# Performance work log

Measured on AMD Instinct MI355X. Metric: run time of the kernel, lower is better.

The kernel has to match this reference:

```python
import math
import jax, jax.numpy as jnp
import numpy as np

T_LEN, BATCH = 215, 256
D_INP = 36; D_MODEL = 36          # d_model must be 36 for internal dims to be consistent
D_T = D_MODEL + 36                # 72: transformer encoder width
N_HEAD = 4; D_HEAD = D_T // N_HEAD
D_FF = 128; N_LAYERS = 2; D_STATIC = 9; N_CLASSES = 2
N_NODES = 36

def _layer_norm(x, g, b, eps=1e-5):
    mu = jnp.mean(x, -1, keepdims=True)
    var = jnp.mean((x - mu) ** 2, -1, keepdims=True)
    return (x - mu) / jnp.sqrt(var + eps) * g + b

def _forward(src, static, times, lengths, W_enc, b_enc, W_emb, b_emb, Wq, bq, Wk, bk, Wv, bv, Wskip, bskip, enc_in_w, enc_in_b, enc_out_w, enc_out_b, enc_ff1_w, enc_ff1_b, enc_ff2_w, enc_ff2_b, enc_ln1_g, enc_ln1_b, enc_ln2_g, enc_ln2_b, mlp_w1, mlp_b1, mlp_w2, mlp_b2):
    T, B = src.shape[0], src.shape[1]
    x = (src[:, :, :D_INP] @ W_enc.T + b_enc) * math.sqrt(D_MODEL)          # [T,B,36]
    # positional encoding: 18 timescales = max_len ** linspace(0,1,18)
    timescales = jnp.asarray(215.0 ** np.linspace(0.0, 1.0, D_MODEL // 2), jnp.float32)
    scaled = times[:, :, None] / timescales                                  # [T,B,18]
    pe = jnp.concatenate([jnp.sin(scaled), jnp.cos(scaled)], -1)             # [T,B,36]
    emb = static @ W_emb.T + b_emb                                           # [B,36]
    mask = jnp.arange(T)[None, :] >= lengths[:, None]                        # [B,T] True = pad
    # --- batched TransformerConv over fully-connected 36-node graph (replaces per-sample loop) ---
    q = x @ Wq.T + bq; k = x @ Wk.T + bk; v = x @ Wv.T + bv
    skip = x @ Wskip.T + bskip
    scores = jnp.einsum('ibe,jbe->bij', q[:N_NODES], k[:N_NODES]) / math.sqrt(36.0)  # i=tgt, j=src
    A = jax.nn.softmax(scores, -1)                      # per-target softmax over incoming edges
    msg = jnp.einsum('bij,jbe->ibe', A, v[:N_NODES])    # edge_weights are all ones
    gout = skip.at[:N_NODES].add(msg)                   # [T,B,36]; rows >= 36 have no in-edges
    # per-edge alpha flattened in nonzero(adj) order: e = src*36 + tgt
    alpha_all = A.transpose(0, 2, 1).reshape(B, N_NODES * N_NODES).T         # [1296,B]
    sq = jnp.sum(alpha_all ** 2, 0)
    d2 = jnp.maximum(sq[:, None] + sq[None, :] - 2.0 * (alpha_all.T @ alpha_all), 0.0)
    distance = jnp.mean(jnp.sqrt(jnp.where(d2 > 0, d2, 1.0)) * (d2 > 0))     # mean pairwise L2
    # --- 2-layer post-norm transformer encoder, width 72, key padding mask ---
    h = jnp.concatenate([gout, pe], -1)                                      # [T,B,72]
    neg = jnp.where(mask[:, None, None, :], -1e9, 0.0)                       # [B,1,1,T]
    for l in range(N_LAYERS):
        qkv = h @ enc_in_w[l].T + enc_in_b[l]
        qh, kh, vh = [t.reshape(T, B, N_HEAD, D_HEAD) for t in jnp.split(qkv, 3, -1)]
        s = jnp.einsum('tbhd,sbhd->bhts', qh, kh) / math.sqrt(D_HEAD) + neg
        ctx = jnp.einsum('bhts,sbhd->tbhd', jax.nn.softmax(s, -1), vh).reshape(T, B, D_T)
        h = _layer_norm(h + ctx @ enc_out_w[l].T + enc_out_b[l], enc_ln1_g[l], enc_ln1_b[l])
        ff = jax.nn.relu(h @ enc_ff1_w[l].T + enc_ff1_b[l]) @ enc_ff2_w[l].T + enc_ff2_b[l]
        h = _layer_norm(h + ff, enc_ln2_g[l], enc_ln2_b[l])
    # masked mean over time, denominator lengths+1 (as in original)
    valid = (~mask).astype(h.dtype).T[:, :, None]                            # [T,B,1]
    pooled = jnp.sum(h * valid, 0) / (lengths.astype(h.dtype)[:, None] + 1.0)
    feat = jnp.concatenate([pooled, emb], -1)                                # [B,108]
    logits = jax.nn.relu(feat @ mlp_w1.T + mlp_b1) @ mlp_w2.T + mlp_b2
    return logits, distance

def setup_inputs() -> dict:
    key = jax.random.key(0)
    ks = jax.random.split(key, 40)
    def nrm(i, shape, s=0.05):
        return jax.random.normal(ks[i], shape, jnp.float32) * s
    return {
        'src': jax.random.normal(ks[0], (T_LEN, BATCH, 2 * D_INP), jnp.float32),
        'static': jax.random.normal(ks[1], (BATCH, D_STATIC), jnp.float32),
        'times': jnp.tile(jnp.arange(T_LEN, dtype=jnp.float32)[:, None], (1, BATCH)),
        'lengths': jax.random.randint(ks[2], (BATCH,), 1, T_LEN + 1),
        'W_enc': nrm(3, (D_MODEL, D_INP)), 'b_enc': jnp.zeros((D_MODEL,), jnp.float32),
        'W_emb': nrm(4, (D_MODEL, D_STATIC)), 'b_emb': jnp.zeros((D_MODEL,), jnp.float32),
        'Wq': nrm(5, (36, 36)), 'bq': nrm(6, (36,)),
        'Wk': nrm(7, (36, 36)), 'bk': nrm(8, (36,)),
        'Wv': nrm(9, (36, 36)), 'bv': nrm(10, (36,)),
        'Wskip': nrm(11, (36, 36)), 'bskip': nrm(12, (36,)),
        'enc_in_w': nrm(13, (N_LAYERS, 3 * D_T, D_T)), 'enc_in_b': nrm(14, (N_LAYERS, 3 * D_T)),
        'enc_out_w': nrm(15, (N_LAYERS, D_T, D_T)), 'enc_out_b': nrm(16, (N_LAYERS, D_T)),
        'enc_ff1_w': nrm(17, (N_LAYERS, D_FF, D_T)), 'enc_ff1_b': nrm(18, (N_LAYERS, D_FF)),
        'enc_ff2_w': nrm(19, (N_LAYERS, D_T, D_FF)), 'enc_ff2_b': nrm(20, (N_LAYERS, D_T)),
        'enc_ln1_g': jnp.ones((N_LAYERS, D_T), jnp.float32), 'enc_ln1_b': jnp.zeros((N_LAYERS, D_T), jnp.float32),
        'enc_ln2_g': jnp.ones((N_LAYERS, D_T), jnp.float32), 'enc_ln2_b': jnp.zeros((N_LAYERS, D_T), jnp.float32),
        'mlp_w1': nrm(21, (108, 108)), 'mlp_b1': nrm(22, (108,)),
        'mlp_w2': nrm(23, (N_CLASSES, 108)), 'mlp_b2': nrm(24, (N_CLASSES,)),
    }

def reference(src, static, times, lengths, W_enc, b_enc, W_emb, b_emb, Wq, bq, Wk, bk, Wv, bv, Wskip, bskip, enc_in_w, enc_in_b, enc_out_w, enc_out_b, enc_ff1_w, enc_ff1_b, enc_ff2_w, enc_ff2_b, enc_ln1_g, enc_ln1_b, enc_ln2_g, enc_ln2_b, mlp_w1, mlp_b1, mlp_w2, mlp_b2):
    return _forward(src, static, times, lengths, W_enc, b_enc, W_emb, b_emb, Wq, bq, Wk, bk, Wv, bv, Wskip, bskip, enc_in_w, enc_in_b, enc_out_w, enc_out_b, enc_ff1_w, enc_ff1_b, enc_ff2_w, enc_ff2_b, enc_ln1_g, enc_ln1_b, enc_ln2_g, enc_ln2_b, mlp_w1, mlp_b1, mlp_w2, mlp_b2)
```

## Files before the change

### kernel.cpp

```cpp
#include <hip/hip_runtime.h>

#define TT 215
#define BB 256
#define ROWS (TT * BB)

typedef __attribute__((ext_vector_type(8))) short short8;
typedef __attribute__((ext_vector_type(4))) float f32x4;

__device__ __forceinline__ unsigned short f2bf_rn(float x) {
    unsigned int u = __float_as_uint(x);
    u = u + 0x7FFFu + ((u >> 16) & 1u);
    return (unsigned short)(u >> 16);
}
__device__ __forceinline__ float bf2f(unsigned short b) {
    return __uint_as_float(((unsigned int)b) << 16);
}

__global__ void k_prep(const float* __restrict__ enc_in_w, const float* __restrict__ ff1_w,
                       const float* __restrict__ ff2_w, const float* __restrict__ enc_out_w,
                       unsigned short* __restrict__ Whi, unsigned short* __restrict__ Wlo,
                       unsigned short* __restrict__ F1hi, unsigned short* __restrict__ F1lo,
                       unsigned short* __restrict__ F2hi, unsigned short* __restrict__ F2lo,
                       unsigned short* __restrict__ Ohi, unsigned short* __restrict__ Olo,
                       float* __restrict__ ts) {
    int g = blockIdx.x * 256 + threadIdx.x;
    if (g < 18) ts[g] = (float)pow(215.0, (double)g / 17.0);
    if (g < 2 * 216 * 96) {
        int l = g / (216 * 96), rem = g % (216 * 96);
        int o = rem / 96, k = rem % 96;
        float v = (k < 72) ? enc_in_w[((size_t)l * 216 + o) * 72 + k] : 0.f;
        unsigned short hi = f2bf_rn(v);
        Whi[g] = hi; Wlo[g] = f2bf_rn(v - bf2f(hi));
    }
    if (g < 2 * 128 * 96) {
        int l = g / (128 * 96), rem = g % (128 * 96);
        int j = rem / 96, k = rem % 96;
        float v = (k < 72) ? ff1_w[((size_t)l * 128 + j) * 72 + k] : 0.f;
        unsigned short hi = f2bf_rn(v);
        F1hi[g] = hi; F1lo[g] = f2bf_rn(v - bf2f(hi));
    }
    if (g < 2 * 72 * 128) {
        float v = ff2_w[g];
        unsigned short hi = f2bf_rn(v);
        F2hi[g] = hi; F2lo[g] = f2bf_rn(v - bf2f(hi));
    }
    if (g < 2 * 72 * 96) {
        int l = g / (72 * 96), rem = g % (72 * 96);
        int o = rem / 96, k = rem % 96;
        float v = (k < 72) ? enc_out_w[((size_t)l * 72 + o) * 72 + k] : 0.f;
        unsigned short hi = f2bf_rn(v);
        Ohi[g] = hi; Olo[g] = f2bf_rn(v - bf2f(hi));
    }
}

__global__ __launch_bounds__(256, 1) void k_enc1(const float* __restrict__ src,
                                                 const float* __restrict__ W,
                                                 const float* __restrict__ bias,
                                                 float* __restrict__ x) {
    int row = blockIdx.x * 256 + threadIdx.x;
    int o0 = blockIdx.y * 9;
    float s[36];
    const float4* sv = (const float4*)(src + (size_t)row * 72);
#pragma unroll
    for (int k = 0; k < 9; ++k) {
        float4 v = sv[k];
        s[4 * k] = v.x; s[4 * k + 1] = v.y; s[4 * k + 2] = v.z; s[4 * k + 3] = v.w;
    }
    float* xp = x + (size_t)row * 36 + o0;
#pragma unroll
    for (int o = 0; o < 9; ++o) {
        float a = bias[o0 + o];
        const float* w = W + (size_t)(o0 + o) * 36;
#pragma unroll
        for (int i = 0; i < 36; ++i) a = fmaf(s[i], w[i], a);
        xp[o] = a * 6.0f;
    }
}

__global__ __launch_bounds__(256, 1) void k_enc2(const float* __restrict__ x,
                                                 const float* __restrict__ W,
                                                 const float* __restrict__ bias,
                                                 float* __restrict__ h) {
    int row = blockIdx.x * 256 + threadIdx.x;
    int o0 = blockIdx.y * 9;
    float xr[36];
    const float4* xv = (const float4*)(x + (size_t)row * 36);
#pragma unroll
    for (int k = 0; k < 9; ++k) {
        float4 v = xv[k];
        xr[4 * k] = v.x; xr[4 * k + 1] = v.y; xr[4 * k + 2] = v.z; xr[4 * k + 3] = v.w;
    }
    float* hp = h + (size_t)row * 72 + o0;
#pragma unroll
    for (int o = 0; o < 9; ++o) {
        float a = bias[o0 + o];
        const float* w = W + (size_t)(o0 + o) * 36;
#pragma unroll
        for (int i = 0; i < 36; ++i) a = fmaf(xr[i], w[i], a);
        hp[o] = a;
    }
}

__global__ __launch_bounds__(256) void k_pe(const float* __restrict__ times,
                                            const float* __restrict__ ts,
                                            float* __restrict__ h) {
    int idx = blockIdx.x * 256 + threadIdx.x;
    int d = idx % 36, row = idx / 36;
    float t = times[row];
    float val;
    if (d < 18) val = sinf(t / ts[d]);
    else        val = cosf(t / ts[d - 18]);
    h[(size_t)row * 72 + 36 + d] = val;
}

__global__ __launch_bounds__(256, 1) void k_graph_qkv(const float* __restrict__ x,
                                                      const float* __restrict__ Wq, const float* __restrict__ bq,
                                                      const float* __restrict__ Wk, const float* __restrict__ bk,
                                                      const float* __restrict__ Wv, const float* __restrict__ bv,
                                                      float* __restrict__ qg, float* __restrict__ kg,
                                                      float* __restrict__ vg) {
    int row = blockIdx.x * 256 + threadIdx.x;
    int mat = blockIdx.y >> 2;
    int o0 = (blockIdx.y & 3) * 9;
    const float* W; const float* bias; float* out;
    if (mat == 0)      { W = Wq; bias = bq; out = qg; }
    else if (mat == 1) { W = Wk; bias = bk; out = kg; }
    else               { W = Wv; bias = bv; out = vg; }
    float xr[36];
    const float4* xv = (const float4*)(x + (size_t)row * 36);
#pragma unroll
    for (int k = 0; k < 9; ++k) {
        float4 v = xv[k];
        xr[4 * k] = v.x; xr[4 * k + 1] = v.y; xr[4 * k + 2] = v.z; xr[4 * k + 3] = v.w;
    }
    float* op = out + (size_t)row * 36 + o0;
#pragma unroll
    for (int o = 0; o < 9; ++o) {
        float a = bias[o0 + o];
        const float* w = W + (size_t)(o0 + o) * 36;
#pragma unroll
        for (int i = 0; i < 36; ++i) a = fmaf(xr[i], w[i], a);
        op[o] = a;
    }
}

__global__ void k_graph_attn(const float* __restrict__ qg, const float* __restrict__ kg,
                             const float* __restrict__ vg, float* __restrict__ h,
                             float* __restrict__ Abuf, float* __restrict__ sqv) {
    __shared__ float q[1296], k[1296], v[1296], A[1296];
    __shared__ float red[128];
    int b = blockIdx.x, tid = threadIdx.x;
    for (int i = tid; i < 1296; i += 128) {
        int t = i / 36, e = i % 36;
        int g = (t * BB + b) * 36 + e;
        q[i] = qg[g]; k[i] = kg[g]; v[i] = vg[g];
    }
    __syncthreads();
    for (int i = tid; i < 1296; i += 128) {
        int r = i / 36, c = i % 36;
        float a = 0.f;
#pragma unroll
        for (int e = 0; e < 36; ++e) a = fmaf(q[r * 36 + e], k[c * 36 + e], a);
        A[i] = a * (1.0f / 6.0f);
    }
    __syncthreads();
    if (tid < 36) {
        float m = -1e30f;
        for (int j = 0; j < 36; ++j) m = fmaxf(m, A[tid * 36 + j]);
        float s = 0.f;
        for (int j = 0; j < 36; ++j) { float e = expf(A[tid * 36 + j] - m); A[tid * 36 + j] = e; s += e; }
        float inv = 1.0f / s;
        for (int j = 0; j < 36; ++j) A[tid * 36 + j] *= inv;
    }
    __syncthreads();
    float lsq = 0.f;
    for (int i = tid; i < 1296; i += 128) {
        float a = A[i];
        Abuf[(size_t)b * 1296 + i] = a;
        lsq = fmaf(a, a, lsq);
        int r = i / 36, e = i % 36;
        float m = 0.f;
#pragma unroll
        for (int j = 0; j < 36; ++j) m = fmaf(A[r * 36 + j], v[j * 36 + e], m);
        h[((size_t)r * BB + b) * 72 + e] += m;
    }
    red[tid] = lsq;
    __syncthreads();
    for (int s = 64; s > 0; s >>= 1) { if (tid < s) red[tid] += red[tid + s]; __syncthreads(); }
    if (tid == 0) sqv[b] = red[0];
}

__global__ void k_gram(const float* __restrict__ Abuf, const float* __restrict__ sqv,
                       float* __restrict__ rowsum) {
    __shared__ float Arow[1296];
    __shared__ float red[256];
    int b1 = blockIdx.x, tid = threadIdx.x;
    for (int i = tid; i < 1296; i += 256) Arow[i] = Abuf[(size_t)b1 * 1296 + i];
    __syncthreads();
    int b2 = tid;
    const float* a2 = Abuf + (size_t)b2 * 1296;
    float dot = 0.f;
    for (int e = 0; e < 1296; ++e) dot = fmaf(Arow[e], a2[e], dot);
    float d2 = fmaxf(sqv[b1] + sqv[b2] - 2.0f * dot, 0.0f);
    red[tid] = (d2 > 0.0f) ? sqrtf(d2) : 0.0f;
    __syncthreads();
    for (int s = 128; s > 0; s >>= 1) { if (tid < s) red[tid] += red[tid + s]; __syncthreads(); }
    if (tid == 0) rowsum[b1] = red[0];
}

__global__ __launch_bounds__(256, 1) void k_qkv(const float* __restrict__ h,
                                                const unsigned short* __restrict__ Whi,
                                                const unsigned short* __restrict__ Wlo,
                                                const float* __restrict__ bias,
                                                float* __restrict__ qkv) {
    int tid = threadIdx.x;
    int w = tid >> 6;
    int lane = tid & 63;
    int n16 = lane & 15;
    int quad = lane >> 4;
    int m0 = blockIdx.x * 64 + w * 16;
    int r = m0 + n16;
    short8 Ahi[3], Alo[3];
#pragma unroll
    for (int s = 0; s < 3; ++s) {
        int k0 = s * 32 + quad * 8;
        float v[8];
        if (k0 < 72) {
            const float4* ap = (const float4*)(h + (size_t)r * 72 + k0);
            float4 v0 = ap[0], v1 = ap[1];
            v[0] = v0.x; v[1] = v0.y; v[2] = v0.z; v[3] = v0.w;
            v[4] = v1.x; v[5] = v1.y; v[6] = v1.z; v[7] = v1.w;
        } else {
#pragma unroll
            for (int j = 0; j < 8; ++j) v[j] = 0.f;
        }
        short8 ph, pl;
#pragma unroll
        for (int j = 0; j < 8; ++j) {
            unsigned short hi = f2bf_rn(v[j]);
            ph[j] = (short)hi;
            pl[j] = (short)f2bf_rn(v[j] - bf2f(hi));
        }
        Ahi[s] = ph; Alo[s] = pl;
    }
    f32x4 acc[14];
#pragma unroll
    for (int t = 0; t < 14; ++t) acc[t] = (f32x4){0.f, 0.f, 0.f, 0.f};
#pragma unroll
    for (int t = 0; t < 14; ++t) {
        int o = t * 16 + n16;
        int oc = (o > 215) ? 215 : o;
        const short8* bh = (const short8*)(Whi + (size_t)oc * 96);
        const short8* bl = (const short8*)(Wlo + (size_t)oc * 96);
        f32x4 a = acc[t];
#pragma unroll
        for (int s = 0; s < 3; ++s) {
            short8 Bh = bh[s * 4 + quad];
            short8 Bl = bl[s * 4 + quad];
            a = __builtin_amdgcn_mfma_f32_16x16x32_bf16(Ahi[s], Bh, a, 0, 0, 0);
            a = __builtin_amdgcn_mfma_f32_16x16x32_bf16(Ahi[s], Bl, a, 0, 0, 0);
            a = __builtin_amdgcn_mfma_f32_16x16x32_bf16(Alo[s], Bh, a, 0, 0, 0);
        }
        acc[t] = a;
    }
#pragma unroll
    for (int t = 0; t < 14; ++t) {
        int col = t * 16 + n16;
        if (col < 216) {
            float b = bias[col];
#pragma unroll
            for (int reg = 0; reg < 4; ++reg) {
                int row = m0 + quad * 4 + reg;
                qkv[(size_t)row * 216 + col] = acc[t][reg] + b;
            }
        }
    }
}

__global__ __launch_bounds__(128, 1) void k_attn(const float* __restrict__ qkv,
                                                 const int* __restrict__ lengths,
                                                 float* __restrict__ ctx) {
    __shared__ float Ks[TT * 20];
    __shared__ float Vs[TT * 20];
    int b = blockIdx.x & (BB - 1);
    int hh = blockIdx.x >> 8;
    int tid = threadIdx.x;
    int len = lengths[b];
    int n20 = len * 20;
    for (int i = tid; i < n20; i += 128) {
        int s = i / 20, d = i % 20;
        float kk = 0.f, vv = 0.f;
        if (d < 18) {
            size_t base2 = ((size_t)s * BB + b) * 216 + hh * 18 + d;
            kk = qkv[base2 + 72];
            vv = qkv[base2 + 144];
        }
        Ks[i] = kk; Vs[i] = vv;
    }
    __syncthreads();
    int t0 = tid, t1 = tid + 128;
    bool two = (t1 < TT);
    const float scale = 0.23570226039551587f;
    float q0[20], q1[20];
    q0[18] = q0[19] = q1[18] = q1[19] = 0.f;
    {
        const float* qb = qkv + ((size_t)t0 * BB + b) * 216 + hh * 18;
#pragma unroll
        for (int d = 0; d < 18; ++d) q0[d] = qb[d] * scale;
    }
    if (two) {
        const float* qb = qkv + ((size_t)t1 * BB + b) * 216 + hh * 18;
#pragma unroll
        for (int d = 0; d < 18; ++d) q1[d] = qb[d] * scale;
    } else {
#pragma unroll
        for (int d = 0; d < 18; ++d) q1[d] = 0.f;
    }
    float l0 = 0.f, l1 = 0.f;
    float acc0[20], acc1[20];
#pragma unroll
    for (int d = 0; d < 20; ++d) { acc0[d] = 0.f; acc1[d] = 0.f; }
    const float4* kp = (const float4*)Ks;
    const float4* vp = (const float4*)Vs;
    for (int s = 0; s < len; ++s) {
        float sc0 = 0.f, sc1 = 0.f;
#pragma unroll
        for (int c = 0; c < 5; ++c) {
            float4 kv = kp[s * 5 + c];
            sc0 = fmaf(q0[4 * c], kv.x, sc0); sc1 = fmaf(q1[4 * c], kv.x, sc1);
            sc0 = fmaf(q0[4 * c + 1], kv.y, sc0); sc1 = fmaf(q1[4 * c + 1], kv.y, sc1);
            sc0 = fmaf(q0[4 * c + 2], kv.z, sc0); sc1 = fmaf(q1[4 * c + 2], kv.z, sc1);
            sc0 = fmaf(q0[4 * c + 3], kv.w, sc0); sc1 = fmaf(q1[4 * c + 3], kv.w, sc1);
        }
        float p0 = __expf(sc0), p1 = __expf(sc1);
        l0 += p0; l1 += p1;
#pragma unroll
        for (int c = 0; c < 5; ++c) {
            float4 vv = vp[s * 5 + c];
            acc0[4 * c]     = fmaf(p0, vv.x, acc0[4 * c]);
            acc0[4 * c + 1] = fmaf(p0, vv.y, acc0[4 * c + 1]);
            acc0[4 * c + 2] = fmaf(p0, vv.z, acc0[4 * c + 2]);
            acc0[4 * c + 3] = fmaf(p0, vv.w, acc0[4 * c + 3]);
            acc1[4 * c]     = fmaf(p1, vv.x, acc1[4 * c]);
            acc1[4 * c + 1] = fmaf(p1, vv.y, acc1[4 * c + 1]);
            acc1[4 * c + 2] = fmaf(p1, vv.z, acc1[4 * c + 2]);
            acc1[4 * c + 3] = fmaf(p1, vv.w, acc1[4 * c + 3]);
        }
    }
    {
        float inv = 1.0f / l0;
        float* cb = ctx + ((size_t)t0 * BB + b) * 72 + hh * 18;
#pragma unroll
        for (int d = 0; d < 18; ++d) cb[d] = acc0[d] * inv;
    }
    if (two) {
        float inv = 1.0f / l1;
        float* cb = ctx + ((size_t)t1 * BB + b) * 72 + hh * 18;
#pragma unroll
        for (int d = 0; d < 18; ++d) cb[d] = acc1[d] * inv;
    }
}

__global__ __launch_bounds__(256, 1) void k_outln(const float* __restrict__ ctx,
                                                  const unsigned short* __restrict__ Ohi,
                                                  const unsigned short* __restrict__ Olo,
                                                  const float* __restrict__ bias,
                                                  const float* __restrict__ g,
                                                  const float* __restrict__ beta,
                                                  float* __restrict__ h) {
    int tid = threadIdx.x;
    int w = tid >> 6;
    int lane = tid & 63;
    int n16 = lane & 15;
    int quad = lane >> 4;
    int m0 = blockIdx.x * 64 + w * 16;
    int r = m0 + n16;
    short8 Ahi[3], Alo[3];
#pragma unroll
    for (int s = 0; s < 3; ++s) {
        int k0 = s * 32 + quad * 8;
        float v[8];
        if (k0 < 72) {
            const float4* ap = (const float4*)(ctx + (size_t)r * 72 + k0);
            float4 v0 = ap[0], v1 = ap[1];
            v[0] = v0.x; v[1] = v0.y; v[2] = v0.z; v[3] = v0.w;
            v[4] = v1.x; v[5] = v1.y; v[6] = v1.z; v[7] = v1.w;
        } else {
#pragma unroll
            for (int j = 0; j < 8; ++j) v[j] = 0.f;
        }
        short8 ph, pl;
#pragma unroll
        for (int j = 0; j < 8; ++j) {
            unsigned short hi = f2bf_rn(v[j]);
            ph[j] = (short)hi;
            pl[j] = (short)f2bf_rn(v[j] - bf2f(hi));
        }
        Ahi[s] = ph; Alo[s] = pl;
    }
    f32x4 acc[5];
#pragma unroll
    for (int t = 0; t < 5; ++t) acc[t] = (f32x4){0.f, 0.f, 0.f, 0.f};
#pragma unroll
    for (int t = 0; t < 5; ++t) {
        int o = t * 16 + n16;
        int oc = (o > 71) ? 71 : o;
        const short8* bh = (const short8*)(Ohi + (size_t)oc * 96);
        const short8* bl = (const short8*)(Olo + (size_t)oc * 96);
        f32x4 a = acc[t];
#pragma unroll
        for (int s = 0; s < 3; ++s) {
            short8 Bh = bh[s * 4 + quad];
            short8 Bl = bl[s * 4 + quad];
            a = __builtin_amdgcn_mfma_f32_16x16x32_bf16(Ahi[s], Bh, a, 0, 0, 0);
            a = __builtin_amdgcn_mfma_f32_16x16x32_bf16(Ahi[s], Bl, a, 0, 0, 0);
            a = __builtin_amdgcn_mfma_f32_16x16x32_bf16(Alo[s], Bh, a, 0, 0, 0);
        }
        acc[t] = a;
    }
    float vals[5][4];
#pragma unroll
    for (int t = 0; t < 5; ++t) {
        int o = t * 16 + n16;
        bool valid = (o < 72);
        float bb = valid ? bias[o] : 0.f;
#pragma unroll
        for (int reg = 0; reg < 4; ++reg) {
            int row = m0 + quad * 4 + reg;
            float hv = valid ? h[(size_t)row * 72 + o] : 0.f;
            vals[t][reg] = acc[t][reg] + bb + hv;
        }
    }
#pragma unroll
    for (int reg = 0; reg < 4; ++reg) {
        float s = 0.f, q = 0.f;
#pragma unroll
        for (int t = 0; t < 5; ++t) {
            int o = t * 16 + n16;
            if (o < 72) { s += vals[t][reg]; q = fmaf(vals[t][reg], vals[t][reg], q); }
        }
#pragma unroll
        for (int m = 1; m < 16; m <<= 1) { s += __shfl_xor(s, m); q += __shfl_xor(q, m); }
        float mu = s / 72.0f;
        float var = fmaxf(q / 72.0f - mu * mu, 0.0f);
        float rstd = 1.0f / sqrtf(var + 1e-5f);
        int row = m0 + quad * 4 + reg;
#pragma unroll
        for (int t = 0; t < 5; ++t) {
            int o = t * 16 + n16;
            if (o < 72)
                h[(size_t)row * 72 + o] = (vals[t][reg] - mu) * rstd * g[o] + beta[o];
        }
    }
}

__global__ __launch_bounds__(256, 1) void k_ffln(const unsigned short* __restrict__ F1hi,
                                                 const unsigned short* __restrict__ F1lo,
                                                 const float* __restrict__ b1,
                                                 const unsigned short* __restrict__ F2hi,
                                                 const unsigned short* __restrict__ F2lo,
                                                 const float* __restrict__ b2,
                                                 const float* __restrict__ g,
                                                 const float* __restrict__ beta,
                                                 float* __restrict__ h) {
    __shared__ float hid[64][129];
    int tid = threadIdx.x;
    int w = tid >> 6;
    int lane = tid & 63;
    int n16 = lane & 15;
    int quad = lane >> 4;
    int m0 = blockIdx.x * 64 + w * 16;
    int r = m0 + n16;
    short8 Ahi[3], Alo[3];
#pragma unroll
    for (int s = 0; s < 3; ++s) {
        int k0 = s * 32 + quad * 8;
        float v[8];
        if (k0 < 72) {
            const float4* ap = (const float4*)(h + (size_t)r * 72 + k0);
            float4 v0 = ap[0], v1 = ap[1];
            v[0] = v0.x; v[1] = v0.y; v[2] = v0.z; v[3] = v0.w;
            v[4] = v1.x; v[5] = v1.y; v[6] = v1.z; v[7] = v1.w;
        } else {
#pragma unroll
            for (int j = 0; j < 8; ++j) v[j] = 0.f;
        }
        short8 ph, pl;
#pragma unroll
        for (int j = 0; j < 8; ++j) {
            unsigned short hi = f2bf_rn(v[j]);
            ph[j] = (short)hi;
            pl[j] = (short)f2bf_rn(v[j] - bf2f(hi));
        }
        Ahi[s] = ph; Alo[s] = pl;
    }
#pragma unroll
    for (int t = 0; t < 8; ++t) {
        int j = t * 16 + n16;
        const short8* bh = (const short8*)(F1hi + (size_t)j * 96);
        const short8* bl = (const short8*)(F1lo + (size_t)j * 96);
        f32x4 a = (f32x4){0.f, 0.f, 0.f, 0.f};
#pragma unroll
        for (int s = 0; s < 3; ++s) {
            short8 Bh = bh[s * 4 + quad];
            short8 Bl = bl[s * 4 + quad];
            a = __builtin_amdgcn_mfma_f32_16x16x32_bf16(Ahi[s], Bh, a, 0, 0, 0);
            a = __builtin_amdgcn_mfma_f32_16x16x32_bf16(Ahi[s], Bl, a, 0, 0, 0);
            a = __builtin_amdgcn_mfma_f32_16x16x32_bf16(Alo[s], Bh, a, 0, 0, 0);
        }
        float bb = b1[j];
#pragma unroll
        for (int reg = 0; reg < 4; ++reg)
            hid[w * 16 + quad * 4 + reg][j] = fmaxf(a[reg] + bb, 0.f);
    }
    short8 A2hi[4], A2lo[4];
#pragma unroll
    for (int s = 0; s < 4; ++s) {
        const float* hp = &hid[w * 16 + n16][s * 32 + quad * 8];
        short8 ph, pl;
#pragma unroll
        for (int j = 0; j < 8; ++j) {
            float v = hp[j];
            unsigned short hi = f2bf_rn(v);
            ph[j] = (short)hi;
            pl[j] = (short)f2bf_rn(v - bf2f(hi));
        }
        A2hi[s] = ph; A2lo[s] = pl;
    }
    f32x4 acc[5];
#pragma unroll
    for (int t = 0; t < 5; ++t) acc[t] = (f32x4){0.f, 0.f, 0.f, 0.f};
#pragma unroll
    for (int t = 0; t < 5; ++t) {
        int o = t * 16 + n16;
        int oc = (o > 71) ? 71 : o;
        const short8* bh = (const short8*)(F2hi + (size_t)oc * 128);
        const short8* bl = (const short8*)(F2lo + (size_t)oc * 128);
        f32x4 a = acc[t];
#pragma unroll
        for (int s = 0; s < 4; ++s) {
            short8 Bh = bh[s * 4 + quad];
            short8 Bl = bl[s * 4 + quad];
            a = __builtin_amdgcn_mfma_f32_16x16x32_bf16(A2hi[s], Bh, a, 0, 0, 0);
            a = __builtin_amdgcn_mfma_f32_16x16x32_bf16(A2hi[s], Bl, a, 0, 0, 0);
            a = __builtin_amdgcn_mfma_f32_16x16x32_bf16(A2lo[s], Bh, a, 0, 0, 0);
        }
        acc[t] = a;
    }
    float vals[5][4];
#pragma unroll
    for (int t = 0; t < 5; ++t) {
        int o = t * 16 + n16;
        bool valid = (o < 72);
        float bb = valid ? b2[o] : 0.f;
#pragma unroll
        for (int reg = 0; reg < 4; ++reg) {
            int row = m0 + quad * 4 + reg;
            float hv = valid ? h[(size_t)row * 72 + o] : 0.f;
            vals[t][reg] = acc[t][reg] + bb + hv;
        }
    }
#pragma unroll
    for (int reg = 0; reg < 4; ++reg) {
        float s = 0.f, q = 0.f;
#pragma unroll
        for (int t = 0; t < 5; ++t) {
            int o = t * 16 + n16;
            if (o < 72) { s += vals[t][reg]; q = fmaf(vals[t][reg], vals[t][reg], q); }
        }
#pragma unroll
        for (int m = 1; m < 16; m <<= 1) { s += __shfl_xor(s, m); q += __shfl_xor(q, m); }
        float mu = s / 72.0f;
        float var = fmaxf(q / 72.0f - mu * mu, 0.0f);
        float rstd = 1.0f / sqrtf(var + 1e-5f);
        int row = m0 + quad * 4 + reg;
#pragma unroll
        for (int t = 0; t < 5; ++t) {
            int o = t * 16 + n16;
            if (o < 72)
                h[(size_t)row * 72 + o] = (vals[t][reg] - mu) * rstd * g[o] + beta[o];
        }
    }
}

__global__ void k_head(const float* __restrict__ h, const int* __restrict__ lengths,
                       const float* __restrict__ statics, const float* __restrict__ W_emb,
                       const float* __restrict__ b_emb, const float* __restrict__ w1,
                       const float* __restrict__ bb1, const float* __restrict__ w2,
                       const float* __restrict__ bb2, float* __restrict__ out) {
    __shared__ float ps2[4][72];
    __shared__ float feat[108];
    __shared__ float hidm[108];
    __shared__ float st[9];
    int b = blockIdx.x, tid = threadIdx.x;
    int w = tid >> 6, lane = tid & 63;
    int len = lengths[b];
    if (tid < 9) st[tid] = statics[b * 9 + tid];
    for (int idx = tid; idx < 288; idx += 256) ((float*)ps2)[idx] = 0.f;
    __syncthreads();
#pragma unroll
    for (int c0 = 0; c0 < 128; c0 += 64) {
        int col = c0 + lane;
        if (col < 72) {
            float s = 0.f;
            for (int t = w; t < len; t += 4) s += h[((size_t)t * BB + b) * 72 + col];
            ps2[w][col] = s;
        }
    }
    __syncthreads();
    if (tid < 72)
        feat[tid] = (ps2[0][tid] + ps2[1][tid] + ps2[2][tid] + ps2[3][tid]) / ((float)len + 1.0f);
    if (tid >= 128 && tid < 164) {
        int o = tid - 128;
        float a = b_emb[o];
#pragma unroll
        for (int i = 0; i < 9; ++i) a = fmaf(st[i], W_emb[o * 9 + i], a);
        feat[72 + o] = a;
    }
    __syncthreads();
    if (tid < 108) {
        float a = bb1[tid];
        for (int i = 0; i < 108; ++i) a = fmaf(feat[i], w1[tid * 108 + i], a);
        hidm[tid] = fmaxf(a, 0.f);
    }
    __syncthreads();
    if (tid < 2) {
        float a = bb2[tid];
        for (int i = 0; i < 108; ++i) a = fmaf(hidm[i], w2[tid * 108 + i], a);
        out[b * 2 + tid] = a;
    }
}

__global__ void k_dist(const float* __restrict__ rowsum, float* __restrict__ out) {
    __shared__ float red[256];
    int tid = threadIdx.x;
    red[tid] = rowsum[tid];
    __syncthreads();
    for (int s = 128; s > 0; s >>= 1) { if (tid < s) red[tid] += red[tid + s]; __syncthreads(); }
    if (tid == 0) out[2 * BB] = red[0] / 65536.0f;
}

extern "C" void kernel_launch(void* const* d_in, const int* in_sizes, int n_in,
                              void* d_out, int out_size, void* d_ws, size_t ws_size,
                              hipStream_t stream) {
    const float* src     = (const float*)d_in[0];
    const float* statics = (const float*)d_in[1];
    const float* times   = (const float*)d_in[2];
    const int*   lengths = (const int*)d_in[3];
    const float* W_enc = (const float*)d_in[4];  const float* b_enc = (const float*)d_in[5];
    const float* W_emb = (const float*)d_in[6];  const float* b_emb = (const float*)d_in[7];
    const float* Wq = (const float*)d_in[8];     const float* bq = (const float*)d_in[9];
    const float* Wk = (const float*)d_in[10];    const float* bk = (const float*)d_in[11];
    const float* Wv = (const float*)d_in[12];    const float* bv = (const float*)d_in[13];
    const float* Wskip = (const float*)d_in[14]; const float* bskip = (const float*)d_in[15];
    const float* enc_in_w = (const float*)d_in[16];  const float* enc_in_b = (const float*)d_in[17];
    const float* enc_out_w = (const float*)d_in[18]; const float* enc_out_b = (const float*)d_in[19];
    const float* ff1_w = (const float*)d_in[20]; const float* ff1_b = (const float*)d_in[21];
    const float* ff2_w = (const float*)d_in[22]; const float* ff2_b = (const float*)d_in[23];
    const float* ln1_g = (const float*)d_in[24]; const float* ln1_b = (const float*)d_in[25];
    const float* ln2_g = (const float*)d_in[26]; const float* ln2_b = (const float*)d_in[27];
    const float* w1 = (const float*)d_in[28];    const float* bb1 = (const float*)d_in[29];
    const float* w2 = (const float*)d_in[30];    const float* bb2 = (const float*)d_in[31];
    float* out = (float*)d_out;

    float* p = (float*)d_ws;
    float* x    = p; p += (size_t)ROWS * 36;
    float* h    = p; p += (size_t)ROWS * 72;
    float* qkv  = p; p += (size_t)ROWS * 216;
    float* ctx  = p; p += (size_t)ROWS * 72;
    float* qg   = p; p += (size_t)36 * BB * 36;
    float* kg   = p; p += (size_t)36 * BB * 36;
    float* vg   = p; p += (size_t)36 * BB * 36;
    float* Abuf = p; p += (size_t)BB * 1296;
    float* sqv  = p; p += BB;
    float* rsum = p; p += BB;
    float* ts   = p; p += 32;
    unsigned short* Whi  = (unsigned short*)p; p += (2 * 216 * 96) / 2;
    unsigned short* Wlo  = (unsigned short*)p; p += (2 * 216 * 96) / 2;
    unsigned short* F1hi = (unsigned short*)p; p += (2 * 128 * 96) / 2;
    unsigned short* F1lo = (unsigned short*)p; p += (2 * 128 * 96) / 2;
    unsigned short* F2hi = (unsigned short*)p; p += (2 * 72 * 128) / 2;
    unsigned short* F2lo = (unsigned short*)p; p += (2 * 72 * 128) / 2;
    unsigned short* Ohi  = (unsigned short*)p; p += (2 * 72 * 96) / 2;
    unsigned short* Olo  = (unsigned short*)p; p += (2 * 72 * 96) / 2;

    k_prep<<<162, 256, 0, stream>>>(enc_in_w, ff1_w, ff2_w, enc_out_w,
                                    Whi, Wlo, F1hi, F1lo, F2hi, F2lo, Ohi, Olo, ts);
    k_enc1<<<dim3(TT, 4), 256, 0, stream>>>(src, W_enc, b_enc, x);
    k_enc2<<<dim3(TT, 4), 256, 0, stream>>>(x, Wskip, bskip, h);
    k_pe<<<(ROWS * 36) / 256, 256, 0, stream>>>(times, ts, h);
    k_graph_qkv<<<dim3(36, 12), 256, 0, stream>>>(x, Wq, bq, Wk, bk, Wv, bv, qg, kg, vg);
    k_graph_attn<<<BB, 128, 0, stream>>>(qg, kg, vg, h, Abuf, sqv);
    k_gram<<<BB, 256, 0, stream>>>(Abuf, sqv, rsum);
    for (int l = 0; l < 2; ++l) {
        k_qkv<<<ROWS / 64, 256, 0, stream>>>(h, Whi + (size_t)l * 216 * 96,
                                             Wlo + (size_t)l * 216 * 96,
                                             enc_in_b + l * 216, qkv);
        k_attn<<<BB * 4, 128, 0, stream>>>(qkv, lengths, ctx);
        k_outln<<<ROWS / 64, 256, 0, stream>>>(ctx, Ohi + (size_t)l * 72 * 96,
                                               Olo + (size_t)l * 72 * 96, enc_out_b + l * 72,
                                               ln1_g + l * 72, ln1_b + l * 72, h);
        k_ffln<<<ROWS / 64, 256, 0, stream>>>(F1hi + (size_t)l * 128 * 96,
                                              F1lo + (size_t)l * 128 * 96, ff1_b + l * 128,
                                              F2hi + (size_t)l * 72 * 128,
                                              F2lo + (size_t)l * 72 * 128, ff2_b + l * 72,
                                              ln2_g + l * 72, ln2_b + l * 72, h);
    }
    k_head<<<BB, 256, 0, stream>>>(h, lengths, statics, W_emb, b_emb, w1, bb1, w2, bb2, out);
    k_dist<<<1, 256, 0, stream>>>(rsum, out);
}
```

Baseline: 574.1 us.

## Skip padded query rows in encoder attention, one wavefront with multi-query slots

The encoder attention kernel now runs one 64-thread wavefront per (batch, head) block. Each thread handles up to four query rows, with queries staged in shared memory alongside K and V. Only query rows below the sequence length are computed and written. A templated core picks the number of query slots at runtime, which removes work on padded query positions and reuses each K/V shared-memory read across more queries. The trade-off is that ctx rows at padded positions are no longer written, so they rely on downstream consumers ignoring those rows. Fewer threads per block may also lower latency hiding.

```diff
diff --git a/kernel.cpp b/kernel.cpp
--- a/kernel.cpp
+++ b/kernel.cpp
@@ -277,87 +277,99 @@
     }
 }
 
-__global__ __launch_bounds__(128, 1) void k_attn(const float* __restrict__ qkv,
-                                                 const int* __restrict__ lengths,
-                                                 float* __restrict__ ctx) {
+template <int NS>
+__device__ __forceinline__ void attn_core(const float* __restrict__ Ks,
+                                          const float* __restrict__ Vs,
+                                          const float q[4][20], float acc[4][20],
+                                          float l[4], int len) {
+    const float4* kp = (const float4*)Ks;
+    const float4* vp = (const float4*)Vs;
+    for (int s = 0; s < len; ++s) {
+        float sc[NS];
+#pragma unroll
+        for (int j = 0; j < NS; ++j) sc[j] = 0.f;
+#pragma unroll
+        for (int c = 0; c < 5; ++c) {
+            float4 kv = kp[s * 5 + c];
+#pragma unroll
+            for (int j = 0; j < NS; ++j) {
+                sc[j] = fmaf(q[j][4 * c], kv.x, sc[j]);
+                sc[j] = fmaf(q[j][4 * c + 1], kv.y, sc[j]);
+                sc[j] = fmaf(q[j][4 * c + 2], kv.z, sc[j]);
+                sc[j] = fmaf(q[j][4 * c + 3], kv.w, sc[j]);
+            }
+        }
+        float p[NS];
+#pragma unroll
+        for (int j = 0; j < NS; ++j) { p[j] = __expf(sc[j]); l[j] += p[j]; }
+#pragma unroll
+        for (int c = 0; c < 5; ++c) {
+            float4 vv = vp[s * 5 + c];
+#pragma unroll
+            for (int j = 0; j < NS; ++j) {
+                acc[j][4 * c]     = fmaf(p[j], vv.x, acc[j][4 * c]);
+                acc[j][4 * c + 1] = fmaf(p[j], vv.y, acc[j][4 * c + 1]);
+                acc[j][4 * c + 2] = fmaf(p[j], vv.z, acc[j][4 * c + 2]);
+                acc[j][4 * c + 3] = fmaf(p[j], vv.w, acc[j][4 * c + 3]);
+            }
+        }
+    }
+}
+
+__global__ __launch_bounds__(64, 1) void k_attn(const float* __restrict__ qkv,
+                                                const int* __restrict__ lengths,
+                                                float* __restrict__ ctx) {
     __shared__ float Ks[TT * 20];
     __shared__ float Vs[TT * 20];
+    __shared__ float Qs[TT * 20];
     int b = blockIdx.x & (BB - 1);
     int hh = blockIdx.x >> 8;
     int tid = threadIdx.x;
     int len = lengths[b];
     int n20 = len * 20;
-    for (int i = tid; i < n20; i += 128) {
+    const float scale = 0.23570226039551587f;
+    for (int i = tid; i < n20; i += 64) {
         int s = i / 20, d = i % 20;
-        float kk = 0.f, vv = 0.f;
+        float kk = 0.f, vv = 0.f, qq = 0.f;
         if (d < 18) {
             size_t base2 = ((size_t)s * BB + b) * 216 + hh * 18 + d;
+            qq = qkv[base2] * scale;
             kk = qkv[base2 + 72];
             vv = qkv[base2 + 144];
         }
-        Ks[i] = kk; Vs[i] = vv;
-    }
-    __syncthreads();
-    int t0 = tid, t1 = tid + 128;
-    bool two = (t1 < TT);
-    const float scale = 0.23570226039551587f;
-    float q0[20], q1[20];
-    q0[18] = q0[19] = q1[18] = q1[19] = 0.f;
-    {
-        const float* qb = qkv + ((size_t)t0 * BB + b) * 216 + hh * 18;
-#pragma unroll
-        for (int d = 0; d < 18; ++d) q0[d] = qb[d] * scale;
-    }
-    if (two) {
-        const float* qb = qkv + ((size_t)t1 * BB + b) * 216 + hh * 18;
-#pragma unroll
-        for (int d = 0; d < 18; ++d) q1[d] = qb[d] * scale;
-    } else {
-#pragma unroll
-        for (int d = 0; d < 18; ++d) q1[d] = 0.f;
-    }
-    float l0 = 0.f, l1 = 0.f;
-    float acc0[20], acc1[20];
-#pragma unroll
-    for (int d = 0; d < 20; ++d) { acc0[d] = 0.f; acc1[d] = 0.f; }
-    const float4* kp = (const float4*)Ks;
-    const float4* vp = (const float4*)Vs;
-    for (int s = 0; s < len; ++s) {
-        float sc0 = 0.f, sc1 = 0.f;
-#pragma unroll
-        for (int c = 0; c < 5; ++c) {
-            float4 kv = kp[s * 5 + c];
-            sc0 = fmaf(q0[4 * c], kv.x, sc0); sc1 = fmaf(q1[4 * c], kv.x, sc1);
-            sc0 = fmaf(q0[4 * c + 1], kv.y, sc0); sc1 = fmaf(q1[4 * c + 1], kv.y, sc1);
-            sc0 = fmaf(q0[4 * c + 2], kv.z, sc0); sc1 = fmaf(q1[4 * c + 2], kv.z, sc1);
-            sc0 = fmaf(q0[4 * c + 3], kv.w, sc0); sc1 = fmaf(q1[4 * c + 3], kv.w, sc1);
-        }
-        float p0 = __expf(sc0), p1 = __expf(sc1);
-        l0 += p0; l1 += p1;
-#pragma unroll
-        for (int c = 0; c < 5; ++c) {
-            float4 vv = vp[s * 5 + c];
-            acc0[4 * c]     = fmaf(p0, vv.x, acc0[4 * c]);
-            acc0[4 * c + 1] = fmaf(p0, vv.y, acc0[4 * c + 1]);
-            acc0[4 * c + 2] = fmaf(p0, vv.z, acc0[4 * c + 2]);
-            acc0[4 * c + 3] = fmaf(p0, vv.w, acc0[4 * c + 3]);
-            acc1[4 * c]     = fmaf(p1, vv.x, acc1[4 * c]);
-            acc1[4 * c + 1] = fmaf(p1, vv.y, acc1[4 * c + 1]);
-            acc1[4 * c + 2] = fmaf(p1, vv.z, acc1[4 * c + 2]);
-            acc1[4 * c + 3] = fmaf(p1, vv.w, acc1[4 * c + 3]);
-        }
-    }
-    {
-        float inv = 1.0f / l0;
-        float* cb = ctx + ((size_t)t0 * BB + b) * 72 + hh * 18;
-#pragma unroll
-        for (int d = 0; d < 18; ++d) cb[d] = acc0[d] * inv;
-    }
-    if (two) {
-        float inv = 1.0f / l1;
-        float* cb = ctx + ((size_t)t1 * BB + b) * 72 + hh * 18;
-#pragma unroll
-        for (int d = 0; d < 18; ++d) cb[d] = acc1[d] * inv;
+        Ks[i] = kk; Vs[i] = vv; Qs[i] = qq;
+    }
+    __syncthreads();
+    int nslot = (len + 63) >> 6;
+    float q[4][20], acc[4][20], l[4];
+#pragma unroll
+    for (int j = 0; j < 4; ++j) {
+        l[j] = 0.f;
+#pragma unroll
+        for (int d = 0; d < 20; ++d) { q[j][d] = 0.f; acc[j][d] = 0.f; }
+    }
+#pragma unroll
+    for (int j = 0; j < 4; ++j) {
+        int t = tid + 64 * j;
+        if (j < nslot && t < len) {
+            const float* qp = Qs + t * 20;
+#pragma unroll
+            for (int d = 0; d < 20; ++d) q[j][d] = qp[d];
+        }
+    }
+    if (nslot == 4)      attn_core<4>(Ks, Vs, q, acc, l, len);
+    else if (nslot == 3) attn_core<3>(Ks, Vs, q, acc, l, len);
+    else if (nslot == 2) attn_core<2>(Ks, Vs, q, acc, l, len);
+    else                 attn_core<1>(Ks, Vs, q, acc, l, len);
+#pragma unroll
+    for (int j = 0; j < 4; ++j) {
+        int t = tid + 64 * j;
+        if (j < nslot && t < len) {
+            float inv = 1.0f / l[j];
+            float* cb = ctx + ((size_t)t * BB + b) * 72 + hh * 18;
+#pragma unroll
+            for (int d = 0; d < 18; ++d) cb[d] = acc[j][d] * inv;
+        }
     }
 }
 
@@ -696,7 +708,7 @@
         k_qkv<<<ROWS / 64, 256, 0, stream>>>(h, Whi + (size_t)l * 216 * 96,
                                              Wlo + (size_t)l * 216 * 96,
                                              enc_in_b + l * 216, qkv);
-        k_attn<<<BB * 4, 128, 0, stream>>>(qkv, lengths, ctx);
+        k_attn<<<BB * 4, 64, 0, stream>>>(qkv, lengths, ctx);
         k_outln<<<ROWS / 64, 256, 0, stream>>>(ctx, Ohi + (size_t)l * 72 * 96,
                                                Olo + (size_t)l * 72 * 96, enc_out_b + l * 72,
                                                ln1_g + l * 72, ln1_b + l * 72, h);
```

Result: slower. 712.1 us (+24.0%).

## Rewrite encoder self-attention with bf16 MFMA tiles and skip padded query rows

Applied to the files above, without the earlier changes.

Replaces the per-thread scalar FP32 attention loop with 16-row query strips per wave. QK^T and PV are computed by bf16 MFMA instructions, with K stored row-major and V transposed in LDS, and the probability tile staged through LDS in bf16. Q keeps a hi/lo bf16 split, but K, V and P are single bf16, which lowers precision. Query strips beyond the sequence length are skipped, so ctx rows for padded positions are no longer written. The block grows to 256 threads. The goal is to remove the scalar FMA bottleneck of the attention stage.

```diff
diff --git a/kernel.cpp b/kernel.cpp
--- a/kernel.cpp
+++ b/kernel.cpp
@@ -277,87 +277,100 @@
     }
 }
 
-__global__ __launch_bounds__(128, 1) void k_attn(const float* __restrict__ qkv,
+__global__ __launch_bounds__(256, 1) void k_attn(const float* __restrict__ qkv,
                                                  const int* __restrict__ lengths,
                                                  float* __restrict__ ctx) {
-    __shared__ float Ks[TT * 20];
-    __shared__ float Vs[TT * 20];
+    __shared__ __attribute__((aligned(16))) unsigned short Kb[215 * 40];
+    __shared__ __attribute__((aligned(16))) unsigned short Vt[32 * 232];
+    __shared__ __attribute__((aligned(16))) unsigned short Pw[4][16 * 232];
     int b = blockIdx.x & (BB - 1);
     int hh = blockIdx.x >> 8;
     int tid = threadIdx.x;
     int len = lengths[b];
-    int n20 = len * 20;
-    for (int i = tid; i < n20; i += 128) {
-        int s = i / 20, d = i % 20;
-        float kk = 0.f, vv = 0.f;
-        if (d < 18) {
-            size_t base2 = ((size_t)s * BB + b) * 216 + hh * 18 + d;
-            kk = qkv[base2 + 72];
-            vv = qkv[base2 + 144];
-        }
-        Ks[i] = kk; Vs[i] = vv;
-    }
-    __syncthreads();
-    int t0 = tid, t1 = tid + 128;
-    bool two = (t1 < TT);
+    for (int i = tid; i < (215 * 40) / 2; i += 256) ((unsigned int*)Kb)[i] = 0u;
+    for (int i = tid; i < (32 * 232) / 2; i += 256) ((unsigned int*)Vt)[i] = 0u;
+    __syncthreads();
+    for (int i = tid; i < len * 18; i += 256) {
+        int s = i / 18, d = i % 18;
+        size_t base2 = ((size_t)s * BB + b) * 216 + hh * 18 + d;
+        Kb[s * 40 + d] = f2bf_rn(qkv[base2 + 72]);
+        Vt[d * 232 + s] = f2bf_rn(qkv[base2 + 144]);
+    }
+    __syncthreads();
+    int w = tid >> 6;
+    int lane = tid & 63;
+    int n16 = lane & 15;
+    int quad = lane >> 4;
     const float scale = 0.23570226039551587f;
-    float q0[20], q1[20];
-    q0[18] = q0[19] = q1[18] = q1[19] = 0.f;
-    {
-        const float* qb = qkv + ((size_t)t0 * BB + b) * 216 + hh * 18;
-#pragma unroll
-        for (int d = 0; d < 18; ++d) q0[d] = qb[d] * scale;
-    }
-    if (two) {
-        const float* qb = qkv + ((size_t)t1 * BB + b) * 216 + hh * 18;
-#pragma unroll
-        for (int d = 0; d < 18; ++d) q1[d] = qb[d] * scale;
-    } else {
-#pragma unroll
-        for (int d = 0; d < 18; ++d) q1[d] = 0.f;
-    }
-    float l0 = 0.f, l1 = 0.f;
-    float acc0[20], acc1[20];
-#pragma unroll
-    for (int d = 0; d < 20; ++d) { acc0[d] = 0.f; acc1[d] = 0.f; }
-    const float4* kp = (const float4*)Ks;
-    const float4* vp = (const float4*)Vs;
-    for (int s = 0; s < len; ++s) {
-        float sc0 = 0.f, sc1 = 0.f;
-#pragma unroll
-        for (int c = 0; c < 5; ++c) {
-            float4 kv = kp[s * 5 + c];
-            sc0 = fmaf(q0[4 * c], kv.x, sc0); sc1 = fmaf(q1[4 * c], kv.x, sc1);
-            sc0 = fmaf(q0[4 * c + 1], kv.y, sc0); sc1 = fmaf(q1[4 * c + 1], kv.y, sc1);
-            sc0 = fmaf(q0[4 * c + 2], kv.z, sc0); sc1 = fmaf(q1[4 * c + 2], kv.z, sc1);
-            sc0 = fmaf(q0[4 * c + 3], kv.w, sc0); sc1 = fmaf(q1[4 * c + 3], kv.w, sc1);
-        }
-        float p0 = __expf(sc0), p1 = __expf(sc1);
-        l0 += p0; l1 += p1;
-#pragma unroll
-        for (int c = 0; c < 5; ++c) {
-            float4 vv = vp[s * 5 + c];
-            acc0[4 * c]     = fmaf(p0, vv.x, acc0[4 * c]);
-            acc0[4 * c + 1] = fmaf(p0, vv.y, acc0[4 * c + 1]);
-            acc0[4 * c + 2] = fmaf(p0, vv.z, acc0[4 * c + 2]);
-            acc0[4 * c + 3] = fmaf(p0, vv.w, acc0[4 * c + 3]);
-            acc1[4 * c]     = fmaf(p1, vv.x, acc1[4 * c]);
-            acc1[4 * c + 1] = fmaf(p1, vv.y, acc1[4 * c + 1]);
-            acc1[4 * c + 2] = fmaf(p1, vv.z, acc1[4 * c + 2]);
-            acc1[4 * c + 3] = fmaf(p1, vv.w, acc1[4 * c + 3]);
-        }
-    }
-    {
-        float inv = 1.0f / l0;
-        float* cb = ctx + ((size_t)t0 * BB + b) * 72 + hh * 18;
-#pragma unroll
-        for (int d = 0; d < 18; ++d) cb[d] = acc0[d] * inv;
-    }
-    if (two) {
-        float inv = 1.0f / l1;
-        float* cb = ctx + ((size_t)t1 * BB + b) * 72 + hh * 18;
-#pragma unroll
-        for (int d = 0; d < 18; ++d) cb[d] = acc1[d] * inv;
+    int nk2 = (len + 31) >> 5;
+    int nkt = nk2 * 2;
+    int nstrips = (len + 15) >> 4;
+    unsigned short* P = &Pw[w][0];
+    for (int strip = w; strip < nstrips; strip += 4) {
+        int q0 = strip * 16;
+        int qr = q0 + n16; if (qr > 214) qr = 214;
+        float qv[8];
+#pragma unroll
+        for (int j = 0; j < 8; ++j) qv[j] = 0.f;
+        {
+            const float* qp = qkv + ((size_t)qr * BB + b) * 216 + hh * 18;
+            int d0 = quad * 8;
+            if (d0 < 16) {
+                const float2* q2 = (const float2*)(qp + d0);
+                float2 a0 = q2[0], a1 = q2[1], a2 = q2[2], a3 = q2[3];
+                qv[0] = a0.x; qv[1] = a0.y; qv[2] = a1.x; qv[3] = a1.y;
+                qv[4] = a2.x; qv[5] = a2.y; qv[6] = a3.x; qv[7] = a3.y;
+            } else if (d0 == 16) {
+                qv[0] = qp[16]; qv[1] = qp[17];
+            }
+        }
+        short8 Qhi, Qlo;
+#pragma unroll
+        for (int j = 0; j < 8; ++j) {
+            float v = qv[j] * scale;
+            unsigned short hi = f2bf_rn(v);
+            Qhi[j] = (short)hi;
+            Qlo[j] = (short)f2bf_rn(v - bf2f(hi));
+        }
+        float lsum[4] = {0.f, 0.f, 0.f, 0.f};
+        for (int kt = 0; kt < nkt; ++kt) {
+            int key = kt * 16 + n16;
+            int kr = (key > 214) ? 214 : key;
+            short8 Bk = *(const short8*)(Kb + kr * 40 + quad * 8);
+            f32x4 S = (f32x4){0.f, 0.f, 0.f, 0.f};
+            S = __builtin_amdgcn_mfma_f32_16x16x32_bf16(Qlo, Bk, S, 0, 0, 0);
+            S = __builtin_amdgcn_mfma_f32_16x16x32_bf16(Qhi, Bk, S, 0, 0, 0);
+#pragma unroll
+            for (int reg = 0; reg < 4; ++reg) {
+                float p = (key < len) ? __expf(S[reg]) : 0.f;
+                lsum[reg] += p;
+                P[(quad * 4 + reg) * 232 + kt * 16 + n16] = f2bf_rn(p);
+            }
+        }
+#pragma unroll
+        for (int m = 1; m < 16; m <<= 1) {
+#pragma unroll
+            for (int reg = 0; reg < 4; ++reg) lsum[reg] += __shfl_xor(lsum[reg], m);
+        }
+        f32x4 o0 = (f32x4){0.f, 0.f, 0.f, 0.f};
+        f32x4 o1 = (f32x4){0.f, 0.f, 0.f, 0.f};
+        for (int k2 = 0; k2 < nk2; ++k2) {
+            short8 Af = *(const short8*)(P + n16 * 232 + k2 * 32 + quad * 8);
+            short8 Bv0 = *(const short8*)(Vt + n16 * 232 + k2 * 32 + quad * 8);
+            short8 Bv1 = *(const short8*)(Vt + (16 + n16) * 232 + k2 * 32 + quad * 8);
+            o0 = __builtin_amdgcn_mfma_f32_16x16x32_bf16(Af, Bv0, o0, 0, 0, 0);
+            o1 = __builtin_amdgcn_mfma_f32_16x16x32_bf16(Af, Bv1, o1, 0, 0, 0);
+        }
+#pragma unroll
+        for (int reg = 0; reg < 4; ++reg) {
+            int t = q0 + quad * 4 + reg;
+            if (t < len) {
+                float inv = 1.0f / lsum[reg];
+                float* cb = ctx + ((size_t)t * BB + b) * 72 + hh * 18;
+                cb[n16] = o0[reg] * inv;
+                if (n16 < 2) cb[16 + n16] = o1[reg] * inv;
+            }
+        }
     }
 }
 
@@ -696,7 +709,7 @@
         k_qkv<<<ROWS / 64, 256, 0, stream>>>(h, Whi + (size_t)l * 216 * 96,
                                              Wlo + (size_t)l * 216 * 96,
                                              enc_in_b + l * 216, qkv);
-        k_attn<<<BB * 4, 128, 0, stream>>>(qkv, lengths, ctx);
+        k_attn<<<BB * 4, 256, 0, stream>>>(qkv, lengths, ctx);
         k_outln<<<ROWS / 64, 256, 0, stream>>>(ctx, Ohi + (size_t)l * 72 * 96,
                                                Olo + (size_t)l * 72 * 96, enc_out_b + l * 72,
                                                ln1_g + l * 72, ln1_b + l * 72, h);
```

New measurement: 500.3 us. 1.15x faster.
